# Performance work log

Measured on AMD Instinct MI355X. Metric: run time of the kernel, lower is better.

Reference implementation:

```python
import jax, jax.numpy as jnp
import numpy as np

EPS = 1e-5
DIM_HEAD = 64
HEADS = 8

def layernorm(x, gamma, beta):
    mu = jnp.mean(x, axis=-1, keepdims=True)
    var = jnp.var(x, axis=-1, keepdims=True)
    return (x - mu) * jax.lax.rsqrt(var + EPS) * gamma + beta

def setup_inputs() -> dict:
    key = jax.random.key(0)
    ks = jax.random.split(key, 8)
    b, n, dh = 1, 896, 3072       # batch, enformer seq len, enformer_hidden_dim
    c, j, dc = 64, 127, 1024      # num contexts (tracks), context len, context_dim
    inner = HEADS * DIM_HEAD      # 512
    return {
        "embeddings": jax.random.normal(ks[0], (b, n, dh), jnp.float32),
        "context": jax.random.normal(ks[1], (c, j, dc), jnp.float32),
        "context_mask": jax.random.randint(ks[2], (b, j), 0, 2) > 0,
        "q_gamma": jnp.ones((dh,), jnp.float32),
        "q_beta": jnp.zeros((dh,), jnp.float32),
        "kv_gamma": jnp.ones((dc,), jnp.float32),
        "kv_beta": jnp.zeros((dc,), jnp.float32),
        "Wq": jax.random.normal(ks[3], (dh, inner), jnp.float32) * 0.02,
        "Wkv": jax.random.normal(ks[4], (dc, 2 * inner), jnp.float32) * 0.02,
        "null_k": jax.random.normal(ks[5], (inner,), jnp.float32),
        "null_v": jax.random.normal(ks[6], (inner,), jnp.float32),
        "Wo": jax.random.normal(ks[7], (inner, dh), jnp.float32) * 0.02,
        "bo": jnp.zeros((dh,), jnp.float32),
        "Wp": jax.random.normal(jax.random.fold_in(key, 9), (dh, 1), jnp.float32) * 0.02,
        "bp": jnp.zeros((1,), jnp.float32),
    }

def reference(embeddings, context, context_mask, q_gamma, q_beta, kv_gamma, kv_beta,
              Wq, Wkv, null_k, null_v, Wo, bo, Wp, bp):
    h, d = HEADS, DIM_HEAD
    scale = d ** -0.5
    b, n, dh = embeddings.shape
    c = context.shape[0]
    # projections
    q = layernorm(embeddings, q_gamma, q_beta) @ Wq            # (b, n, h*d)
    kv = layernorm(context, kv_gamma, kv_beta) @ Wkv           # (c, j, 2*h*d)
    k, v = jnp.split(kv, 2, axis=-1)
    # prepend null key/value token
    k = jnp.concatenate([jnp.broadcast_to(null_k, (c, 1, h * d)), k], axis=1)
    v = jnp.concatenate([jnp.broadcast_to(null_v, (c, 1, h * d)), v], axis=1)
    # split heads: (b, h, i, d) / (c, h, j, d)
    q = q.reshape(b, n, h, d).transpose(0, 2, 1, 3)
    k = k.reshape(c, -1, h, d).transpose(0, 2, 1, 3)
    v = v.reshape(c, -1, h, d).transpose(0, 2, 1, 3)
    sim = jnp.einsum('bhid,chjd->bchij', q, k) * scale         # (b, c, h, i, j+1)
    # mask: pad with True for the null token, broadcast over c, h, i
    mask = jnp.pad(context_mask, ((0, 0), (1, 0)), constant_values=True)
    sim = jnp.where(mask[:, None, None, None, :], sim, -jnp.finfo(sim.dtype).max)
    attn = jax.nn.softmax(sim, axis=-1)
    out = jnp.einsum('bchij,chjd->bchid', attn, v)             # (b, c, h, i, d)
    out = out.transpose(0, 1, 3, 2, 4).reshape(b, c, n, h * d)  # (b, c, n, h*d)
    branch = out @ Wo + bo                                     # (b, c, n, dh)
    emb = embeddings[:, None] + branch                         # (b, c, n, dh)
    pred = jax.nn.softplus((emb @ Wp + bp)[..., 0])            # (b, c, n)
    return pred.transpose(0, 2, 1)                             # (b, n, c)
```

## Files before the change

kernel.cpp:

```cpp
#include <hip/hip_runtime.h>
#include <math.h>

#define N_SEQ   896
#define DH      3072
#define NCTX    64
#define JLEN    127
#define DC      1024
#define HEADS   8
#define DHEAD   64
#define INNER   512
#define MKV     8128
#define MKVPAD  8192

typedef __bf16 bf16x8 __attribute__((ext_vector_type(8)));
typedef float  f32x4  __attribute__((ext_vector_type(4)));

#define OFF_EDOT   0LL
#define OFF_QBF    (OFF_EDOT + N_SEQ)
#define OFF_KBF    (OFF_QBF  + (long long)N_SEQ*INNER/2)
#define OFF_VPM    (OFF_KBF  + (long long)NCTX*128*INNER/2)
#define OFF_VPNULL (OFF_VPM  + (long long)MKV*8)
#define OFF_WOP    (OFF_VPNULL + 8)
#define OFF_BOP    (OFF_WOP  + INNER)
#define OFF_SBUF   (OFF_BOP  + 16)
#define OFF_ANQ    (OFF_SBUF + (long long)NCTX*HEADS*N_SEQ)
#define OFF_ANKV   (OFF_ANQ  + (long long)N_SEQ*DH/2)
#define OFF_WQT    (OFF_ANKV + (long long)MKVPAD*DC/2)
#define OFF_WKT    (OFF_WQT  + (long long)INNER*DH/2)
#define OFF_WVPT   (OFF_WKT  + (long long)INNER*DC/2)
#define OFF_QSL    (OFF_WVPT + 16*1024/2)

__device__ __forceinline__ void async_copy16(const __bf16* g, __bf16* l) {
    __builtin_amdgcn_global_load_lds(
        (const __attribute__((address_space(1))) unsigned int*)g,
        (__attribute__((address_space(3))) unsigned int*)l,
        16, 0, 0);
}

#define P_KV0  10
#define P_Q0   (P_KV0 + 2032)
#define P_T0   (P_Q0 + 224)
#define GRIDP  (P_T0 + 2048)

__global__ __launch_bounds__(256)
void prep_kernel(const float* __restrict__ emb, const float* __restrict__ ctx,
                 const float* __restrict__ qg, const float* __restrict__ qb_,
                 const float* __restrict__ kvg, const float* __restrict__ kvb,
                 const float* __restrict__ Wq, const float* __restrict__ Wkv,
                 const float* __restrict__ Wo, const float* __restrict__ bo,
                 const float* __restrict__ Wp,
                 const float* __restrict__ nullk, const float* __restrict__ nullv,
                 __bf16* __restrict__ ANQ, __bf16* __restrict__ ANKV,
                 __bf16* __restrict__ WQT, __bf16* __restrict__ WKT,
                 __bf16* __restrict__ WVPT, float* __restrict__ VPNULL,
                 float* __restrict__ EDOT, float* __restrict__ BOP,
                 __bf16* __restrict__ KBF)
{
    __shared__ __align__(16) float SM[3072 + 64];
    const int bid = blockIdx.x, tid = threadIdx.x;
    const int lane = tid & 63, wid = tid >> 6;

    if (bid < 8) {
        int h = bid;
        float* wpsh = SM;
        float* wops = SM + 3072;
        for (int i = tid; i < 768; i += 256)
            ((f32x4*)wpsh)[i] = ((const f32x4*)Wp)[i];
        __syncthreads();
        for (int rr = 0; rr < 16; ++rr) {
            int d = wid * 16 + rr;
            const float* worow = Wo + (long long)(h * 64 + d) * DH;
            float s = 0.f;
            #pragma unroll
            for (int c = 0; c < 12; ++c) {
                int col = c * 256 + lane * 4;
                float4 a = *(const float4*)&worow[col];
                s += a.x*wpsh[col] + a.y*wpsh[col+1] + a.z*wpsh[col+2] + a.w*wpsh[col+3];
            }
            #pragma unroll
            for (int o = 1; o < 64; o <<= 1) s += __shfl_xor(s, o);
            if (lane == 0) wops[d] = s;
        }
        __syncthreads();
        if (tid < 64) {
            float v = nullv[h * 64 + tid] * wops[tid];
            #pragma unroll
            for (int o = 1; o < 64; o <<= 1) v += __shfl_xor(v, o);
            if (tid == 0) VPNULL[h] = v;
        }
        #pragma unroll
        for (int kk = 0; kk < 4; ++kk) {
            int k = kk * 256 + tid;
            const float* src = Wkv + (long long)k * (2 * INNER) + INNER + h * 64;
            float s2 = 0.f;
            #pragma unroll
            for (int d2 = 0; d2 < 64; d2 += 4) {
                float4 a = *(const float4*)&src[d2];
                s2 += a.x*wops[d2] + a.y*wops[d2+1] + a.z*wops[d2+2] + a.w*wops[d2+3];
            }
            WVPT[h * 1024 + k] = (__bf16)s2;
        }
    } else if (bid == 8) {
        float* red = SM;
        float s = 0.f;
        #pragma unroll
        for (int i = 0; i < 3; ++i) {
            int k = i * 1024 + tid * 4;
            float4 a = *(const float4*)&bo[k];
            float4 w = *(const float4*)&Wp[k];
            s += a.x*w.x + a.y*w.y + a.z*w.z + a.w*w.w;
        }
        #pragma unroll
        for (int o = 1; o < 64; o <<= 1) s += __shfl_xor(s, o);
        if (lane == 0) red[wid] = s;
        __syncthreads();
        if (tid == 0) *BOP = red[0] + red[1] + red[2] + red[3];
    } else if (bid == 9) {
        for (int i = tid; i < 8 * 1024; i += 256)
            WVPT[8 * 1024 + i] = (__bf16)0.f;
        for (int i = tid; i < NCTX * INNER; i += 256) {
            int c = i >> 9, d2 = i & 511;
            KBF[(long long)(c * 128) * INNER + d2] = (__bf16)nullk[d2];
        }
    } else if (bid < P_Q0) {
        int r = (bid - P_KV0) * 4 + wid;
        const float* x = ctx + (long long)r * DC;
        f32x4 xv[4];
        float s = 0.f, ss = 0.f;
        #pragma unroll
        for (int c = 0; c < 4; ++c) {
            const f32x4* p = (const f32x4*)&x[c * 256 + lane * 4];
            xv[c] = __builtin_nontemporal_load(p);
            s  += xv[c][0] + xv[c][1] + xv[c][2] + xv[c][3];
            ss += xv[c][0]*xv[c][0] + xv[c][1]*xv[c][1]
                + xv[c][2]*xv[c][2] + xv[c][3]*xv[c][3];
        }
        #pragma unroll
        for (int o = 1; o < 64; o <<= 1) { s += __shfl_xor(s, o); ss += __shfl_xor(ss, o); }
        float m  = s * (1.f / DC);
        float rs = rsqrtf(ss * (1.f / DC) - m * m + 1e-5f);
        __bf16* op = ANKV + (long long)r * DC;
        #pragma unroll
        for (int c = 0; c < 4; ++c) {
            int col = c * 256 + lane * 4;
            float4 g4 = *(const float4*)&kvg[col];
            float4 b4 = *(const float4*)&kvb[col];
            __bf16 ov[4];
            ov[0] = (__bf16)((xv[c][0] - m) * rs * g4.x + b4.x);
            ov[1] = (__bf16)((xv[c][1] - m) * rs * g4.y + b4.y);
            ov[2] = (__bf16)((xv[c][2] - m) * rs * g4.z + b4.z);
            ov[3] = (__bf16)((xv[c][3] - m) * rs * g4.w + b4.w);
            *(ushort4*)&op[col] = *(ushort4*)ov;
        }
    } else if (bid < P_T0) {
        int r = (bid - P_Q0) * 4 + wid;
        const float* x = emb + (long long)r * DH;
        float s = 0.f, ss = 0.f, dp = 0.f;
        #pragma unroll
        for (int c = 0; c < 12; ++c) {
            int col = c * 256 + lane * 4;
            float4 a = *(const float4*)&x[col];
            float4 w = *(const float4*)&Wp[col];
            s  += a.x + a.y + a.z + a.w;
            ss += a.x*a.x + a.y*a.y + a.z*a.z + a.w*a.w;
            dp += a.x*w.x + a.y*w.y + a.z*w.z + a.w*w.w;
        }
        #pragma unroll
        for (int o = 1; o < 64; o <<= 1) {
            s += __shfl_xor(s, o); ss += __shfl_xor(ss, o); dp += __shfl_xor(dp, o);
        }
        float m  = s * (1.f / DH);
        float rs = rsqrtf(ss * (1.f / DH) - m * m + 1e-5f);
        __bf16* op = ANQ + (long long)r * DH;
        #pragma unroll
        for (int c = 0; c < 12; ++c) {
            int col = c * 256 + lane * 4;
            float4 a  = *(const float4*)&x[col];
            float4 g4 = *(const float4*)&qg[col];
            float4 b4 = *(const float4*)&qb_[col];
            __bf16 ov[4];
            ov[0] = (__bf16)((a.x - m) * rs * g4.x + b4.x);
            ov[1] = (__bf16)((a.y - m) * rs * g4.y + b4.y);
            ov[2] = (__bf16)((a.z - m) * rs * g4.z + b4.z);
            ov[3] = (__bf16)((a.w - m) * rs * g4.w + b4.w);
            *(ushort4*)&op[col] = *(ushort4*)ov;
        }
        if (lane == 0) EDOT[r] = dp;
    } else {
        int t = bid - P_T0;
        float (*tT)[33] = (float(*)[33])SM;
        const float* src; __bf16* dst; int srcS, dstS, rb, cb;
        if (t < 1536) {
            rb = (t >> 4) * 32; cb = (t & 15) * 32;
            src = Wq; srcS = INNER; dst = WQT; dstS = DH;
        } else {
            int bi = t - 1536;
            rb = (bi >> 4) * 32; cb = (bi & 15) * 32;
            src = Wkv; srcS = 2 * INNER; dst = WKT; dstS = DC;
        }
        int tx = tid & 31, ty = tid >> 5;
        #pragma unroll
        for (int i = 0; i < 32; i += 8)
            tT[ty + i][tx] = src[(long long)(rb + ty + i) * srcS + cb + tx];
        __syncthreads();
        #pragma unroll
        for (int i = 0; i < 32; i += 8)
            dst[(long long)(cb + ty + i) * dstS + rb + tx] = (__bf16)tT[tx][ty + i];
    }
}

__global__ __launch_bounds__(256)
void proj_kernel(const __bf16* __restrict__ ANQ, const __bf16* __restrict__ WQT,
                 const __bf16* __restrict__ ANKV, const __bf16* __restrict__ WKT,
                 const __bf16* __restrict__ WVPT,
                 float* __restrict__ qsl, __bf16* __restrict__ kout,
                 float* __restrict__ vpm) {
    __shared__ __align__(16) __bf16 As[128 * 32];
    __shared__ __align__(16) __bf16 Bs[128 * 32];
    int b = blockIdx.x;
    int tid = threadIdx.x;
    int lane = tid & 63, w = tid >> 6;
    int n16 = lane & 15, quad = lane >> 4;
    int wr = (w >> 1) * 64, wc = (w & 1) * 64;

    const __bf16 *A, *B;
    int K, kbeg, kend, mode, slice = 0;
    long long m0, n0;
    if (b < 224) {
        mode = 0; slice = b / 28;
        int rem = b % 28;
        m0 = (long long)(rem % 7) * 128;
        n0 = (long long)(rem / 7) * 128;
        K = DH; kbeg = slice * 384; kend = kbeg + 384;
        A = ANQ; B = WQT;
    } else {
        mode = 1;
        int b2 = b - 224;
        m0 = (long long)(b2 & 63) * 128;
        n0 = (long long)(b2 >> 6) * 128;
        K = DC; kbeg = 0; kend = DC;
        A = ANKV; B = WKT;
    }
    bool dovp = (mode == 1) && (n0 == 0);

    const __bf16* aG = A + (m0 + (tid >> 2)) * K + (tid & 3) * 8;
    const __bf16* bG = B + (n0 + (tid >> 2)) * K + (tid & 3) * 8;
    __bf16* aL = As + tid * 8;
    __bf16* bL = Bs + tid * 8;

    f32x4 acc[4][4], accv[4];
    const f32x4 z = {0.f, 0.f, 0.f, 0.f};
    #pragma unroll
    for (int i = 0; i < 4; ++i) {
        accv[i] = z;
        #pragma unroll
        for (int j = 0; j < 4; ++j) acc[i][j] = z;
    }

    for (int k0 = kbeg; k0 < kend; k0 += 32) {
        async_copy16(aG + k0, aL);
        async_copy16(aG + (long long)64 * K + k0, aL + 2048);
        async_copy16(bG + k0, bL);
        async_copy16(bG + (long long)64 * K + k0, bL + 2048);
        bf16x8 bv;
        if (dovp) bv = *(const bf16x8*)&WVPT[n16 * 1024 + k0 + quad * 8];
        __syncthreads();
        bf16x8 af[4], bfr[4];
        #pragma unroll
        for (int i = 0; i < 4; ++i)
            af[i]  = *(const bf16x8*)&As[(wr + i * 16 + n16) * 32 + quad * 8];
        #pragma unroll
        for (int j = 0; j < 4; ++j)
            bfr[j] = *(const bf16x8*)&Bs[(wc + j * 16 + n16) * 32 + quad * 8];
        #pragma unroll
        for (int i = 0; i < 4; ++i)
            #pragma unroll
            for (int j = 0; j < 4; ++j)
                acc[i][j] = __builtin_amdgcn_mfma_f32_16x16x32_bf16(af[i], bfr[j], acc[i][j], 0, 0, 0);
        if (dovp) {
            #pragma unroll
            for (int i = 0; i < 4; ++i)
                accv[i] = __builtin_amdgcn_mfma_f32_16x16x32_bf16(af[i], bv, accv[i], 0, 0, 0);
        }
        __syncthreads();
    }

    if (mode == 0) {
        float* qdst = qsl + (long long)slice * (N_SEQ * INNER);
        #pragma unroll
        for (int i = 0; i < 4; ++i)
            #pragma unroll
            for (int r = 0; r < 4; ++r) {
                long long gr = m0 + wr + i * 16 + quad * 4 + r;
                #pragma unroll
                for (int j = 0; j < 4; ++j) {
                    long long gc = n0 + wc + j * 16 + n16;
                    qdst[gr * INNER + gc] = acc[i][j][r];
                }
            }
    } else {
        #pragma unroll
        for (int i = 0; i < 4; ++i)
            #pragma unroll
            for (int r = 0; r < 4; ++r) {
                long long gr = m0 + wr + i * 16 + quad * 4 + r;
                if (gr >= MKV) continue;
                int cc = (int)(gr / JLEN), jj = (int)(gr % JLEN);
                #pragma unroll
                for (int j = 0; j < 4; ++j) {
                    long long gc = n0 + wc + j * 16 + n16;
                    kout[((long long)(cc * 128) + jj + 1) * INNER + gc] = (__bf16)acc[i][j][r];
                }
                if (dovp && n16 < 8) vpm[gr * 8 + n16] = accv[i][r];
            }
    }
}

__global__ __launch_bounds__(256)
void qreduce_kernel(const float* __restrict__ qsl, __bf16* __restrict__ qbf) {
    int i = blockIdx.x * 256 + threadIdx.x;
    float4 s4 = {0.f, 0.f, 0.f, 0.f};
    #pragma unroll
    for (int k = 0; k < 8; ++k) {
        float4 a = *(const float4*)&qsl[(long long)k * (N_SEQ * INNER) + i * 4];
        s4.x += a.x; s4.y += a.y; s4.z += a.z; s4.w += a.w;
    }
    __bf16 ov[4] = {(__bf16)s4.x, (__bf16)s4.y, (__bf16)s4.z, (__bf16)s4.w};
    *(ushort4*)&qbf[i * 4] = *(ushort4*)ov;
}

#define KROW 72

__global__ __launch_bounds__(256)
void attn_mfma_kernel(const __bf16* __restrict__ qb, const __bf16* __restrict__ kb,
                      const float* __restrict__ vpm, const float* __restrict__ vpnull,
                      const int* __restrict__ mask, float* __restrict__ s_buf) {
    __shared__ __align__(16) __bf16 ksh[128 * KROW];
    __shared__ float vpsh[128];
    __shared__ float amsh[128];
    int ch = blockIdx.x;
    int h = ch & 7, c = ch >> 3;
    int tid = threadIdx.x;
    int lane = tid & 63, w = tid >> 6;
    int n16 = lane & 15, quad = lane >> 4;

    const __bf16* kbase = kb + (long long)(c * 128) * INNER + h * DHEAD;
    #pragma unroll
    for (int p = 0; p < 4; ++p) {
        int chunk = tid + p * 256;
        int row = chunk >> 3, o = chunk & 7;
        bf16x8 v = *(const bf16x8*)(kbase + (long long)row * INNER + o * 8);
        *(bf16x8*)&ksh[row * KROW + o * 8] = v;
    }
    if (tid < 128) {
        vpsh[tid] = (tid == 0) ? vpnull[h] : vpm[(long long)(c * JLEN + tid - 1) * 8 + h];
        amsh[tid] = (tid == 0) ? 0.f : (mask[tid - 1] ? 0.f : -3.0e38f);
    }
    __syncthreads();

    bf16x8 bF[8][2];
    #pragma unroll
    for (int t = 0; t < 8; ++t)
        #pragma unroll
        for (int s = 0; s < 2; ++s)
            bF[t][s] = *(const bf16x8*)&ksh[(t * 16 + n16) * KROW + s * 32 + quad * 8];

    float vpv[8], am[8];
    #pragma unroll
    for (int t = 0; t < 8; ++t) {
        vpv[t] = vpsh[t * 16 + n16];
        am[t]  = amsh[t * 16 + n16];
    }

    const __bf16* qbase = qb + h * DHEAD;
    const f32x4 zero = {0.f, 0.f, 0.f, 0.f};

    for (int xi = 0; xi < 7; ++xi) {
        bf16x8 aF[2][2];
        int r0s[2];
        #pragma unroll
        for (int it2 = 0; it2 < 2; ++it2) {
            int tile = xi * 8 + it2 * 4 + w;
            r0s[it2] = tile * 16;
            const __bf16* qrow = qbase + (long long)(r0s[it2] + n16) * INNER + quad * 8;
            aF[it2][0] = *(const bf16x8*)(qrow);
            aF[it2][1] = *(const bf16x8*)(qrow + 32);
        }

        #pragma unroll
        for (int it2 = 0; it2 < 2; ++it2) {
            int r0 = r0s[it2];
            f32x4 acc[8];
            #pragma unroll
            for (int t = 0; t < 8; ++t) {
                acc[t] = __builtin_amdgcn_mfma_f32_16x16x32_bf16(aF[it2][0], bF[t][0], zero,   0, 0, 0);
                acc[t] = __builtin_amdgcn_mfma_f32_16x16x32_bf16(aF[it2][1], bF[t][1], acc[t], 0, 0, 0);
            }
            float mloc = -3.0e38f;
            #pragma unroll
            for (int t = 0; t < 8; ++t)
                #pragma unroll
                for (int r = 0; r < 4; ++r)
                    mloc = fmaxf(mloc, acc[t][r] * 0.125f + am[t]);
            #pragma unroll
            for (int o = 1; o < 16; o <<= 1) mloc = fmaxf(mloc, __shfl_xor(mloc, o, 16));
            float lr[4] = {0.f, 0.f, 0.f, 0.f}, pr[4] = {0.f, 0.f, 0.f, 0.f};
            #pragma unroll
            for (int t = 0; t < 8; ++t) {
                #pragma unroll
                for (int r = 0; r < 4; ++r) {
                    float e = __expf(acc[t][r] * 0.125f + am[t] - mloc);
                    lr[r] += e; pr[r] += e * vpv[t];
                }
            }
            #pragma unroll
            for (int o = 1; o < 16; o <<= 1) {
                #pragma unroll
                for (int r = 0; r < 4; ++r) {
                    lr[r] += __shfl_xor(lr[r], o, 16);
                    pr[r] += __shfl_xor(pr[r], o, 16);
                }
            }
            if (n16 == 0) {
                #pragma unroll
                for (int r = 0; r < 4; ++r)
                    s_buf[(long long)ch * N_SEQ + r0 + quad * 4 + r] = pr[r] / lr[r];
            }
        }
    }
}

__global__ void final_kernel(const float* __restrict__ s_buf,
                             const float* __restrict__ e_dot,
                             const float* __restrict__ bop,
                             const float* __restrict__ bp,
                             float* __restrict__ out) {
    int t = blockIdx.x * blockDim.x + threadIdx.x;
    if (t >= N_SEQ * NCTX) return;
    int n = t >> 6, c = t & 63;
    float s = 0.f;
    #pragma unroll
    for (int h = 0; h < HEADS; ++h) s += s_buf[((long long)(c * HEADS + h)) * N_SEQ + n];
    float x = e_dot[n] + s + *bop + *bp;
    out[t] = fmaxf(x, 0.f) + log1pf(__expf(-fabsf(x)));
}

extern "C" void kernel_launch(void* const* d_in, const int* in_sizes, int n_in,
                              void* d_out, int out_size, void* d_ws, size_t ws_size,
                              hipStream_t stream) {
    const float* emb   = (const float*)d_in[0];
    const float* ctx   = (const float*)d_in[1];
    const int*   cmask = (const int*)  d_in[2];
    const float* qg    = (const float*)d_in[3];
    const float* qb_   = (const float*)d_in[4];
    const float* kvg   = (const float*)d_in[5];
    const float* kvb   = (const float*)d_in[6];
    const float* Wq    = (const float*)d_in[7];
    const float* Wkv   = (const float*)d_in[8];
    const float* nullk = (const float*)d_in[9];
    const float* nullv = (const float*)d_in[10];
    const float* Wo    = (const float*)d_in[11];
    const float* bo    = (const float*)d_in[12];
    const float* Wp    = (const float*)d_in[13];
    const float* bp    = (const float*)d_in[14];
    float* out  = (float*)d_out;
    float* ws_f = (float*)d_ws;

    float*  EDOT   = ws_f + OFF_EDOT;
    __bf16* QBF    = (__bf16*)(ws_f + OFF_QBF);
    __bf16* KBF    = (__bf16*)(ws_f + OFF_KBF);
    float*  VPM    = ws_f + OFF_VPM;
    float*  VPNULL = ws_f + OFF_VPNULL;
    float*  BOP    = ws_f + OFF_BOP;
    float*  SBUF   = ws_f + OFF_SBUF;
    __bf16* ANQ    = (__bf16*)(ws_f + OFF_ANQ);
    __bf16* ANKV   = (__bf16*)(ws_f + OFF_ANKV);
    __bf16* WQT    = (__bf16*)(ws_f + OFF_WQT);
    __bf16* WKT    = (__bf16*)(ws_f + OFF_WKT);
    __bf16* WVPT   = (__bf16*)(ws_f + OFF_WVPT);
    float*  QSL    = ws_f + OFF_QSL;

    prep_kernel<<<GRIDP, 256, 0, stream>>>(
        emb, ctx, qg, qb_, kvg, kvb, Wq, Wkv, Wo, bo, Wp, nullk, nullv,
        ANQ, ANKV, WQT, WKT, WVPT, VPNULL, EDOT, BOP, KBF);
    proj_kernel<<<480, 256, 0, stream>>>(ANQ, WQT, ANKV, WKT, WVPT, QSL, KBF, VPM);
    qreduce_kernel<<<(N_SEQ * INNER) / 1024, 256, 0, stream>>>(QSL, QBF);
    attn_mfma_kernel<<<NCTX * HEADS, 256, 0, stream>>>(
        QBF, KBF, VPM, VPNULL, cmask, SBUF);
    final_kernel<<<(N_SEQ * NCTX + 255) / 256, 256, 0, stream>>>(SBUF, EDOT, BOP, bp, out);
}
```

Baseline: 211.7 us.

## Fuse context layernorm apply into KV projection GEMM A-tile loading

The prep kernel now computes only per-row mean and rsqrt statistics for the context instead of writing a normalized bf16 copy. The KV projection kernel reads raw fp32 context, normalizes it with the stored statistics and gamma/beta from shared memory, and writes bf16 into the LDS A tile. This removes the round trip of writing and rereading the normalized context buffer. In exchange, each column block rereads the fp32 context, which is double the bytes of the bf16 copy, and these become synchronous loads rather than async global-to-LDS copies. The attention kernel also raises wave priority around its MFMA block.

```diff
diff --git a/kernel.cpp b/kernel.cpp
--- a/kernel.cpp
+++ b/kernel.cpp
@@ -29,6 +29,7 @@
 #define OFF_WKT    (OFF_WQT  + (long long)INNER*DH/2)
 #define OFF_WVPT   (OFF_WKT  + (long long)INNER*DC/2)
 #define OFF_QSL    (OFF_WVPT + 16*1024/2)
+#define OFF_MRS    (OFF_QSL  + (long long)8*N_SEQ*INNER)
 
 __device__ __forceinline__ void async_copy16(const __bf16* g, __bf16* l) {
     __builtin_amdgcn_global_load_lds(
@@ -38,19 +39,18 @@
 }
 
 #define P_KV0  10
-#define P_Q0   (P_KV0 + 2032)
+#define P_Q0   (P_KV0 + 508)
 #define P_T0   (P_Q0 + 224)
 #define GRIDP  (P_T0 + 2048)
 
 __global__ __launch_bounds__(256)
 void prep_kernel(const float* __restrict__ emb, const float* __restrict__ ctx,
                  const float* __restrict__ qg, const float* __restrict__ qb_,
-                 const float* __restrict__ kvg, const float* __restrict__ kvb,
                  const float* __restrict__ Wq, const float* __restrict__ Wkv,
                  const float* __restrict__ Wo, const float* __restrict__ bo,
                  const float* __restrict__ Wp,
                  const float* __restrict__ nullk, const float* __restrict__ nullv,
-                 __bf16* __restrict__ ANQ, __bf16* __restrict__ ANKV,
+                 __bf16* __restrict__ ANQ, float* __restrict__ MRS,
                  __bf16* __restrict__ WQT, __bf16* __restrict__ WKT,
                  __bf16* __restrict__ WVPT, float* __restrict__ VPNULL,
                  float* __restrict__ EDOT, float* __restrict__ BOP,
@@ -123,34 +123,33 @@
             KBF[(long long)(c * 128) * INNER + d2] = (__bf16)nullk[d2];
         }
     } else if (bid < P_Q0) {
-        int r = (bid - P_KV0) * 4 + wid;
-        const float* x = ctx + (long long)r * DC;
-        f32x4 xv[4];
-        float s = 0.f, ss = 0.f;
-        #pragma unroll
-        for (int c = 0; c < 4; ++c) {
-            const f32x4* p = (const f32x4*)&x[c * 256 + lane * 4];
-            xv[c] = __builtin_nontemporal_load(p);
-            s  += xv[c][0] + xv[c][1] + xv[c][2] + xv[c][3];
-            ss += xv[c][0]*xv[c][0] + xv[c][1]*xv[c][1]
-                + xv[c][2]*xv[c][2] + xv[c][3]*xv[c][3];
-        }
-        #pragma unroll
-        for (int o = 1; o < 64; o <<= 1) { s += __shfl_xor(s, o); ss += __shfl_xor(ss, o); }
-        float m  = s * (1.f / DC);
-        float rs = rsqrtf(ss * (1.f / DC) - m * m + 1e-5f);
-        __bf16* op = ANKV + (long long)r * DC;
-        #pragma unroll
-        for (int c = 0; c < 4; ++c) {
-            int col = c * 256 + lane * 4;
-            float4 g4 = *(const float4*)&kvg[col];
-            float4 b4 = *(const float4*)&kvb[col];
-            __bf16 ov[4];
-            ov[0] = (__bf16)((xv[c][0] - m) * rs * g4.x + b4.x);
-            ov[1] = (__bf16)((xv[c][1] - m) * rs * g4.y + b4.y);
-            ov[2] = (__bf16)((xv[c][2] - m) * rs * g4.z + b4.z);
-            ov[3] = (__bf16)((xv[c][3] - m) * rs * g4.w + b4.w);
-            *(ushort4*)&op[col] = *(ushort4*)ov;
+        int r0 = (bid - P_KV0) * 16 + wid * 4;
+        const float* x = ctx + (long long)r0 * DC;
+        float s[4] = {0.f,0.f,0.f,0.f}, ss[4] = {0.f,0.f,0.f,0.f};
+        #pragma unroll
+        for (int rr = 0; rr < 4; ++rr) {
+            #pragma unroll
+            for (int c = 0; c < 4; ++c) {
+                f32x4 v = *(const f32x4*)&x[(long long)rr * DC + c * 256 + lane * 4];
+                s[rr]  += v[0] + v[1] + v[2] + v[3];
+                ss[rr] += v[0]*v[0] + v[1]*v[1] + v[2]*v[2] + v[3]*v[3];
+            }
+        }
+        #pragma unroll
+        for (int o = 1; o < 64; o <<= 1) {
+            #pragma unroll
+            for (int rr = 0; rr < 4; ++rr) {
+                s[rr] += __shfl_xor(s[rr], o); ss[rr] += __shfl_xor(ss[rr], o);
+            }
+        }
+        if (lane == 0) {
+            #pragma unroll
+            for (int rr = 0; rr < 4; ++rr) {
+                float m  = s[rr] * (1.f / DC);
+                float rs = rsqrtf(ss[rr] * (1.f / DC) - m * m + 1e-5f);
+                MRS[(long long)(r0 + rr) * 2]     = m;
+                MRS[(long long)(r0 + rr) * 2 + 1] = rs;
+            }
         }
     } else if (bid < P_T0) {
         int r = (bid - P_Q0) * 4 + wid;
@@ -211,42 +210,65 @@
 
 __global__ __launch_bounds__(256)
 void proj_kernel(const __bf16* __restrict__ ANQ, const __bf16* __restrict__ WQT,
-                 const __bf16* __restrict__ ANKV, const __bf16* __restrict__ WKT,
-                 const __bf16* __restrict__ WVPT,
+                 const float* __restrict__ ctx, const __bf16* __restrict__ WKT,
+                 const float* __restrict__ kvg, const float* __restrict__ kvb,
+                 const float* __restrict__ MRS, const __bf16* __restrict__ WVPT,
                  float* __restrict__ qsl, __bf16* __restrict__ kout,
                  float* __restrict__ vpm) {
     __shared__ __align__(16) __bf16 As[128 * 32];
     __shared__ __align__(16) __bf16 Bs[128 * 32];
+    __shared__ __align__(16) float gsh[1024];
+    __shared__ __align__(16) float bsh[1024];
+    __shared__ float msh[128], rsh[128];
     int b = blockIdx.x;
     int tid = threadIdx.x;
     int lane = tid & 63, w = tid >> 6;
     int n16 = lane & 15, quad = lane >> 4;
     int wr = (w >> 1) * 64, wc = (w & 1) * 64;
 
-    const __bf16 *A, *B;
+    const __bf16 *B;
     int K, kbeg, kend, mode, slice = 0;
     long long m0, n0;
+    const __bf16* aGq = nullptr;
     if (b < 224) {
         mode = 0; slice = b / 28;
         int rem = b % 28;
         m0 = (long long)(rem % 7) * 128;
         n0 = (long long)(rem / 7) * 128;
         K = DH; kbeg = slice * 384; kend = kbeg + 384;
-        A = ANQ; B = WQT;
+        B = WQT;
+        aGq = ANQ + (m0 + (tid >> 2)) * K + (tid & 3) * 8;
     } else {
         mode = 1;
         int b2 = b - 224;
         m0 = (long long)(b2 & 63) * 128;
         n0 = (long long)(b2 >> 6) * 128;
         K = DC; kbeg = 0; kend = DC;
-        A = ANKV; B = WKT;
+        B = WKT;
+        for (int i = tid; i < 256; i += 256) {
+            ((f32x4*)gsh)[i] = ((const f32x4*)kvg)[i];
+            ((f32x4*)bsh)[i] = ((const f32x4*)kvb)[i];
+        }
+        if (tid < 128) {
+            long long gr = m0 + tid; if (gr >= MKV) gr = MKV - 1;
+            msh[tid] = MRS[gr * 2];
+            rsh[tid] = MRS[gr * 2 + 1];
+        }
+        __syncthreads();
     }
     bool dovp = (mode == 1) && (n0 == 0);
 
-    const __bf16* aG = A + (m0 + (tid >> 2)) * K + (tid & 3) * 8;
     const __bf16* bG = B + (n0 + (tid >> 2)) * K + (tid & 3) * 8;
     __bf16* aL = As + tid * 8;
     __bf16* bL = Bs + tid * 8;
+
+    int ri = tid >> 2, c8 = (tid & 3) * 8;
+    long long r0c = m0 + ri;       if (r0c >= MKV) r0c = MKV - 1;
+    long long r1c = m0 + 64 + ri;  if (r1c >= MKV) r1c = MKV - 1;
+    const float* x0 = ctx + r0c * DC + c8;
+    const float* x1 = ctx + r1c * DC + c8;
+    float mv0 = msh[ri], rv0 = rsh[ri];
+    float mv1 = msh[64 + ri], rv1 = rsh[64 + ri];
 
     f32x4 acc[4][4], accv[4];
     const f32x4 z = {0.f, 0.f, 0.f, 0.f};
@@ -258,8 +280,27 @@
     }
 
     for (int k0 = kbeg; k0 < kend; k0 += 32) {
-        async_copy16(aG + k0, aL);
-        async_copy16(aG + (long long)64 * K + k0, aL + 2048);
+        if (mode == 0) {
+            async_copy16(aGq + k0, aL);
+            async_copy16(aGq + (long long)64 * K + k0, aL + 2048);
+        } else {
+            f32x4 a0 = *(const f32x4*)(x0 + k0);
+            f32x4 a1 = *(const f32x4*)(x0 + k0 + 4);
+            f32x4 c0 = *(const f32x4*)(x1 + k0);
+            f32x4 c1 = *(const f32x4*)(x1 + k0 + 4);
+            const float* gp = &gsh[k0 + c8];
+            const float* bp = &bsh[k0 + c8];
+            __bf16 o0[8], o1[8];
+            #pragma unroll
+            for (int j = 0; j < 4; ++j) {
+                o0[j]     = (__bf16)((a0[j] - mv0) * rv0 * gp[j]     + bp[j]);
+                o0[j + 4] = (__bf16)((a1[j] - mv0) * rv0 * gp[j + 4] + bp[j + 4]);
+                o1[j]     = (__bf16)((c0[j] - mv1) * rv1 * gp[j]     + bp[j]);
+                o1[j + 4] = (__bf16)((c1[j] - mv1) * rv1 * gp[j + 4] + bp[j + 4]);
+            }
+            *(bf16x8*)aL = *(bf16x8*)o0;
+            *(bf16x8*)(aL + 2048) = *(bf16x8*)o1;
+        }
         async_copy16(bG + k0, bL);
         async_copy16(bG + (long long)64 * K + k0, bL + 2048);
         bf16x8 bv;
@@ -391,11 +432,13 @@
         for (int it2 = 0; it2 < 2; ++it2) {
             int r0 = r0s[it2];
             f32x4 acc[8];
+            __builtin_amdgcn_s_setprio(1);
             #pragma unroll
             for (int t = 0; t < 8; ++t) {
                 acc[t] = __builtin_amdgcn_mfma_f32_16x16x32_bf16(aF[it2][0], bF[t][0], zero,   0, 0, 0);
                 acc[t] = __builtin_amdgcn_mfma_f32_16x16x32_bf16(aF[it2][1], bF[t][1], acc[t], 0, 0, 0);
             }
+            __builtin_amdgcn_s_setprio(0);
             float mloc = -3.0e38f;
             #pragma unroll
             for (int t = 0; t < 8; ++t)
@@ -474,16 +517,17 @@
     float*  BOP    = ws_f + OFF_BOP;
     float*  SBUF   = ws_f + OFF_SBUF;
     __bf16* ANQ    = (__bf16*)(ws_f + OFF_ANQ);
-    __bf16* ANKV   = (__bf16*)(ws_f + OFF_ANKV);
     __bf16* WQT    = (__bf16*)(ws_f + OFF_WQT);
     __bf16* WKT    = (__bf16*)(ws_f + OFF_WKT);
     __bf16* WVPT   = (__bf16*)(ws_f + OFF_WVPT);
     float*  QSL    = ws_f + OFF_QSL;
+    float*  MRS    = ws_f + OFF_MRS;
 
     prep_kernel<<<GRIDP, 256, 0, stream>>>(
-        emb, ctx, qg, qb_, kvg, kvb, Wq, Wkv, Wo, bo, Wp, nullk, nullv,
-        ANQ, ANKV, WQT, WKT, WVPT, VPNULL, EDOT, BOP, KBF);
-    proj_kernel<<<480, 256, 0, stream>>>(ANQ, WQT, ANKV, WKT, WVPT, QSL, KBF, VPM);
+        emb, ctx, qg, qb_, Wq, Wkv, Wo, bo, Wp, nullk, nullv,
+        ANQ, MRS, WQT, WKT, WVPT, VPNULL, EDOT, BOP, KBF);
+    proj_kernel<<<480, 256, 0, stream>>>(
+        ANQ, WQT, ctx, WKT, kvg, kvb, MRS, WVPT, QSL, KBF, VPM);
     qreduce_kernel<<<(N_SEQ * INNER) / 1024, 256, 0, stream>>>(QSL, QBF);
     attn_mfma_kernel<<<NCTX * HEADS, 256, 0, stream>>>(
         QBF, KBF, VPM, VPNULL, cmask, SBUF);
```

New measurement: 229.1 us. +8.2%, slower.
